# Optimization experiments

Measured on AMD Instinct MI355X. Metric: run time of the kernel, lower is better.

## Reference

```python
import jax, jax.numpy as jnp
import numpy as np

B, N, F_IN, H, L = 4, 2048, 3, 32, 3
H2 = H // 2


def setup_inputs() -> dict:
    key = jax.random.key(0)
    ks = jax.random.split(key, 16)
    feats = jax.random.normal(ks[0], (B, N, F_IN), dtype=jnp.float32)
    coors = jax.random.normal(ks[1], (B, N, 3), dtype=jnp.float32) * 3.0
    adj = jax.random.randint(ks[2], (B, N, N), 0, 2).astype(bool)
    adj = adj | jnp.eye(N, dtype=bool)[None]  # self-loops so every row has a neighbor
    s = 0.1
    return {
        "feats": feats,
        "coors": coors,
        "adj_mat": adj,
        "W_in": jax.random.normal(ks[3], (F_IN, H), dtype=jnp.float32) * s,
        "Wq": jax.random.normal(ks[4], (L, H, H), dtype=jnp.float32) * s,
        "Wk": jax.random.normal(ks[5], (L, H, H), dtype=jnp.float32) * s,
        "Wv": jax.random.normal(ks[6], (L, H, H), dtype=jnp.float32) * s,
        "Wo": jax.random.normal(ks[7], (L, H, H), dtype=jnp.float32) * s,
        "W1": jax.random.normal(ks[8], (L, H, 2 * H), dtype=jnp.float32) * s,
        "W2": jax.random.normal(ks[9], (L, 2 * H, H), dtype=jnp.float32) * s,
        "coor_scale": jnp.full((L,), 0.1, dtype=jnp.float32),
        "Wf1": jax.random.normal(ks[10], (H, H2), dtype=jnp.float32) * s,
        "bf1": jnp.zeros((H2,), dtype=jnp.float32),
        "Wf2": jax.random.normal(ks[11], (H2, 3), dtype=jnp.float32) * s,
        "bf2": jnp.zeros((3,), dtype=jnp.float32),
    }


def _se3_forward(feats, coors, adj_mat, W_in, Wq, Wk, Wv, Wo, W1, W2, coor_scale):
    h = feats @ W_in                      # [B,N,H]
    x = coors
    neg = jnp.finfo(h.dtype).min
    inv_sqrt_d = 1.0 / jnp.sqrt(jnp.asarray(H, h.dtype))
    for l in range(L):                    # small static layer loop
        rel = x[:, :, None, :] - x[:, None, :, :]          # [B,N,N,3]
        dist2 = jnp.sum(rel * rel, axis=-1)                 # [B,N,N]
        q = h @ Wq[l]
        k = h @ Wk[l]
        v = h @ Wv[l]
        logits = jnp.einsum('bie,bje->bij', q, k) * inv_sqrt_d - dist2
        logits = jnp.where(adj_mat, logits, neg)
        attn = jax.nn.softmax(logits, axis=-1)              # [B,N,N]
        h = h + jnp.einsum('bij,bjd->bid', attn, v) @ Wo[l]
        # equivariant coordinate update (attention-weighted relative vectors)
        x = x + coor_scale[l] * jnp.einsum('bij,bijc->bic', attn, rel)
        h = h + jax.nn.relu(h @ W1[l]) @ W2[l]
    return h


def reference(feats, coors, adj_mat, W_in, Wq, Wk, Wv, Wo, W1, W2,
              coor_scale, Wf1, bf1, Wf2, bf2):
    h = _se3_forward(feats, coors, adj_mat, W_in, Wq, Wk, Wv, Wo, W1, W2, coor_scale)
    pooled = h.mean(axis=1)                                 # [B,H]
    out = jax.nn.relu(pooled @ Wf1 + bf1) @ Wf2 + bf2       # [B,3]
    return out
```

## Files before the change

kernel.cpp:

```cpp
#include <hip/hip_runtime.h>
#include <cstddef>
#include <cstdint>

#define N_     2048
#define H_     32
#define NEGF   (-1.0e30f)
#define LOG2E  1.4426950408889634f
#define C1F    (0.17677669529663687f * 1.4426950408889634f)
#define DEFER  16.0f
#define NCHUNK 32
#define CLEN   64
#define NRTOT  8192
#define PREC   20

#define AS1 __attribute__((address_space(1)))
#define AS3 __attribute__((address_space(3)))

typedef unsigned short ushortT;
typedef short v8s __attribute__((ext_vector_type(8)));
typedef float v4f __attribute__((ext_vector_type(4)));

__device__ __forceinline__ float exp2_fast(float x) {
    float r;
    asm("v_exp_f32 %0, %1" : "=v"(r) : "v"(x));
    return r;
}

__device__ __forceinline__ unsigned f2bf(float x) {
    unsigned u = __builtin_bit_cast(unsigned, x);
    return (u + 0x7FFFu + ((u >> 16) & 1u)) >> 16;
}

__global__ __launch_bounds__(256) void k_adjmask(const int* __restrict__ adj,
                                                 unsigned long long* __restrict__ mask) {
    size_t idx = (size_t)blockIdx.x * 256 + threadIdx.x;
    unsigned long long m = __ballot(adj[idx] != 0);
    if ((threadIdx.x & 63) == 0) mask[idx >> 6] = m;
}

__global__ __launch_bounds__(256) void k_init_qkv(const float* __restrict__ feats,
                                                  const float* __restrict__ W_in,
                                                  const float* __restrict__ Wq,
                                                  const float* __restrict__ Wk,
                                                  const float* __restrict__ Wv,
                                                  float* __restrict__ h,
                                                  ushortT* __restrict__ qb,
                                                  ushortT* __restrict__ kb,
                                                  ushortT* __restrict__ vb) {
    __shared__ float hs[8][33];
    int t = threadIdx.x;
    int rl = t >> 5, c = t & 31;
    int row = blockIdx.x * 8 + rl;
    float f0 = feats[row * 3 + 0], f1 = feats[row * 3 + 1], f2 = feats[row * 3 + 2];
    float hv = f0 * W_in[c] + f1 * W_in[32 + c] + f2 * W_in[64 + c];
    hs[rl][c] = hv;
    h[(row << 5) + c] = hv;
    __syncthreads();
    float aq = 0.f, ak = 0.f, av = 0.f;
#pragma unroll
    for (int d = 0; d < 32; ++d) {
        float hd = hs[rl][d];
        aq += hd * Wq[(d << 5) + c];
        ak += hd * Wk[(d << 5) + c];
        av += hd * Wv[(d << 5) + c];
    }
    qb[(row << 5) + c] = (ushortT)f2bf(aq * C1F);
    kb[(row << 5) + c] = (ushortT)f2bf(ak);
    vb[(row << 5) + c] = (ushortT)f2bf(av);
}

__global__ __launch_bounds__(256) void k_attn(const ushortT* __restrict__ qb,
                                              const ushortT* __restrict__ kb,
                                              const ushortT* __restrict__ vb,
                                              const float* __restrict__ xin,
                                              const unsigned long long* __restrict__ maskg,
                                              float* __restrict__ pm,
                                              float* __restrict__ ps,
                                              unsigned* __restrict__ pacc) {
    __shared__ __attribute__((aligned(16))) ushortT k_lds[64 * 32];
    __shared__ __attribute__((aligned(16))) ushortT vt_lds[32 * 72];
    __shared__ __attribute__((aligned(16))) float4  x_lds[64];
    __shared__ __attribute__((aligned(16))) ushortT p_lds[4][16 * 40];

    const int t = threadIdx.x;
    const int w = t >> 6, l = t & 63;
    const int g = l >> 4, q = l & 15;
    const int rowblk = blockIdx.x >> 5;
    const int cid    = blockIdx.x & 31;
    const int bN = (rowblk >> 5) << 11;
    const int j0 = cid << 6;
    const int rq = rowblk * 64 + w * 16 + q;

    __builtin_amdgcn_global_load_lds(
        (const AS1 void*)((const char*)(kb + (((size_t)(bN + j0)) << 5)) + t * 16),
        (AS3 void*)((char*)k_lds + t * 16), 16, 0, 0);
    {
        const int j = t & 63, grp = t >> 6;
        const uint4 vv = *(const uint4*)(vb + (((size_t)(bN + j0 + j)) << 5) + grp * 8);
        unsigned arr[4] = {vv.x, vv.y, vv.z, vv.w};
#pragma unroll
        for (int ii = 0; ii < 4; ++ii) {
            vt_lds[(grp * 8 + 2 * ii) * 72 + j]     = (ushortT)(arr[ii] & 0xffffu);
            vt_lds[(grp * 8 + 2 * ii + 1) * 72 + j] = (ushortT)(arr[ii] >> 16);
        }
    }
    if (t < 64) {
        const float* xp = xin + ((size_t)(bN + j0 + t)) * 3;
        float4 xv; xv.x = xp[0]; xv.y = xp[1]; xv.z = xp[2]; xv.w = 0.f;
        x_lds[t] = xv;
    }

    const v8s qf = *(const v8s*)(qb + (((size_t)rq) << 5) + g * 8);
    const float xi0 = xin[rq * 3 + 0], xi1 = xin[rq * 3 + 1], xi2 = xin[rq * 3 + 2];
    const unsigned long long mw = maskg[(((size_t)rq) << 5) + cid];

    v4f oA = {0.f, 0.f, 0.f, 0.f}, oB = {0.f, 0.f, 0.f, 0.f};
    float m = NEGF, sum = 0.f;
    float xa0 = 0.f, xa1 = 0.f, xa2 = 0.f;

    __syncthreads();

    ushortT* pw = &p_lds[w][0];

#pragma unroll
    for (int half = 0; half < 2; ++half) {
        const int jt = half * 32;
        v8s kA = *(const v8s*)(k_lds + (jt + q) * 32 + g * 8);
        v8s kB = *(const v8s*)(k_lds + (jt + 16 + q) * 32 + g * 8);
        v4f zero = {0.f, 0.f, 0.f, 0.f};
        v4f sA = __builtin_amdgcn_mfma_f32_16x16x32_bf16(kA, qf, zero, 0, 0, 0);
        v4f sB = __builtin_amdgcn_mfma_f32_16x16x32_bf16(kB, qf, zero, 0, 0, 0);

        float se[8];
        float4 xjA[4], xjB[4];
        float pot = NEGF;
#pragma unroll
        for (int reg = 0; reg < 4; ++reg) {
            const int jA = jt + 4 * g + reg, jB = jA + 16;
            xjA[reg] = x_lds[jA];
            xjB[reg] = x_lds[jB];
            float dA0 = xi0 - xjA[reg].x, dA1 = xi1 - xjA[reg].y, dA2 = xi2 - xjA[reg].z;
            float dB0 = xi0 - xjB[reg].x, dB1 = xi1 - xjB[reg].y, dB2 = xi2 - xjB[reg].z;
            float distA = fmaf(dA2, dA2, fmaf(dA1, dA1, dA0 * dA0));
            float distB = fmaf(dB2, dB2, fmaf(dB1, dB1, dB0 * dB0));
            const int bA = (int)((mw >> jA) & 1ULL);
            const int bB = (int)((mw >> jB) & 1ULL);
            se[reg]     = bA ? fmaf(distA, -LOG2E, sA[reg]) : NEGF;
            se[4 + reg] = bB ? fmaf(distB, -LOG2E, sB[reg]) : NEGF;
            pot = fmaxf(pot, fmaxf(se[reg], se[4 + reg]));
        }
        pot = fmaxf(pot, __shfl_xor(pot, 16));
        pot = fmaxf(pot, __shfl_xor(pot, 32));
        if (__any(pot - m > DEFER)) {
            float n2 = fmaxf(m, pot);
            float al = exp2_fast(m - n2);
            m = n2; sum *= al;
            v4f alv = {al, al, al, al};
            oA *= alv; oB *= alv;
            xa0 *= al; xa1 *= al; xa2 *= al;
        }
        float p[8];
#pragma unroll
        for (int i = 0; i < 8; ++i) { p[i] = exp2_fast(se[i] - m); sum += p[i]; }
#pragma unroll
        for (int reg = 0; reg < 4; ++reg) {
            xa0 = fmaf(p[reg], xjA[reg].x, fmaf(p[4 + reg], xjB[reg].x, xa0));
            xa1 = fmaf(p[reg], xjA[reg].y, fmaf(p[4 + reg], xjB[reg].y, xa1));
            xa2 = fmaf(p[reg], xjA[reg].z, fmaf(p[4 + reg], xjB[reg].z, xa2));
        }
        uint2 wA, wB;
        wA.x = f2bf(p[0]) | (f2bf(p[1]) << 16);
        wA.y = f2bf(p[2]) | (f2bf(p[3]) << 16);
        wB.x = f2bf(p[4]) | (f2bf(p[5]) << 16);
        wB.y = f2bf(p[6]) | (f2bf(p[7]) << 16);
        *(uint2*)(pw + q * 40 + 4 * g)      = wA;
        *(uint2*)(pw + q * 40 + 16 + 4 * g) = wB;
        v8s pf = *(const v8s*)(pw + q * 40 + 8 * g);
        v8s vA = *(const v8s*)(vt_lds + q * 72 + jt + 8 * g);
        v8s vB = *(const v8s*)(vt_lds + (16 + q) * 72 + jt + 8 * g);
        oA = __builtin_amdgcn_mfma_f32_16x16x32_bf16(vA, pf, oA, 0, 0, 0);
        oB = __builtin_amdgcn_mfma_f32_16x16x32_bf16(vB, pf, oB, 0, 0, 0);
    }

    sum += __shfl_xor(sum, 16); sum += __shfl_xor(sum, 32);
    xa0 += __shfl_xor(xa0, 16); xa0 += __shfl_xor(xa0, 32);
    xa1 += __shfl_xor(xa1, 16); xa1 += __shfl_xor(xa1, 32);
    xa2 += __shfl_xor(xa2, 16); xa2 += __shfl_xor(xa2, 32);

    unsigned* pb = pacc + ((size_t)cid * NRTOT + rq) * PREC;
    uint2 rA, rB;
    rA.x = f2bf(oA[0]) | (f2bf(oA[1]) << 16);
    rA.y = f2bf(oA[2]) | (f2bf(oA[3]) << 16);
    rB.x = f2bf(oB[0]) | (f2bf(oB[1]) << 16);
    rB.y = f2bf(oB[2]) | (f2bf(oB[3]) << 16);
    *(uint2*)(pb + 2 * g)     = rA;
    *(uint2*)(pb + 8 + 2 * g) = rB;
    if (g == 0) {
        float4 tl; tl.x = xa0; tl.y = xa1; tl.z = xa2; tl.w = 0.f;
        *(float4*)(pb + 16) = tl;
        pm[(((size_t)rq) << 5) + cid] = m;
        ps[(((size_t)rq) << 5) + cid] = sum;
    }
}

__global__ __launch_bounds__(256) void k_mergefin(const float* __restrict__ pm,
                                                  const float* __restrict__ ps,
                                                  const unsigned* __restrict__ pacc,
                                                  float* __restrict__ hg,
                                                  const float* __restrict__ xin,
                                                  float* __restrict__ xout,
                                                  const float* __restrict__ Wo,
                                                  const float* __restrict__ W1,
                                                  const float* __restrict__ W2,
                                                  const float* __restrict__ csp,
                                                  const float* __restrict__ Wqn,
                                                  const float* __restrict__ Wkn,
                                                  const float* __restrict__ Wvn,
                                                  ushortT* __restrict__ qout,
                                                  ushortT* __restrict__ kout,
                                                  ushortT* __restrict__ vout) {
    __shared__ float wo_s[1024];
    __shared__ float w1_s[2048];
    __shared__ float w2_s[2048];
    __shared__ float wq_s[1024];
    __shared__ float wk_s[1024];
    __shared__ float wv_s[1024];
    __shared__ float ad_s[4][40];
    __shared__ float h1_s[4][36];
    __shared__ float h2_s[4][36];
    __shared__ float f_s[4][64];

    const int t = threadIdx.x, w = t >> 6, lane = t & 63;
    for (int i = t; i < 1024; i += 256) wo_s[i] = Wo[i];
    for (int i = t; i < 2048; i += 256) { w1_s[i] = W1[i]; w2_s[i] = W2[i]; }
    if (Wqn) {
        for (int i = t; i < 1024; i += 256) {
            wq_s[i] = Wqn[i]; wk_s[i] = Wkn[i]; wv_s[i] = Wvn[i];
        }
    }
    __syncthreads();

    const int r = (blockIdx.x << 2) + w;

    float pmv = NEGF, psv = 0.f;
    if (lane < NCHUNK) { pmv = pm[((size_t)r << 5) + lane]; psv = ps[((size_t)r << 5) + lane]; }
    float m_g = pmv;
#pragma unroll
    for (int off = 1; off < 64; off <<= 1) m_g = fmaxf(m_g, __shfl_xor(m_g, off));
    float scv = (lane < NCHUNK) ? exp2_fast(pmv - m_g) : 0.f;
    float sg = scv * psv;
#pragma unroll
    for (int off = 1; off < 64; off <<= 1) sg += __shfl_xor(sg, off);
    const float rinv = 1.0f / sg;

    const int off32 = (lane < 32) ? (lane >> 1) : (16 + ((lane - 32) & 3));
    const bool isTail = lane >= 32;
    const bool hiHalf = lane & 1;
    float ad = 0.f;
#pragma unroll
    for (int c = 0; c < NCHUNK; ++c) {
        float scc = __shfl(scv, c);
        unsigned u = pacc[((size_t)c * NRTOT + r) * PREC + off32];
        float f = isTail ? __builtin_bit_cast(float, u)
                         : __builtin_bit_cast(float, hiHalf ? (u & 0xffff0000u) : (u << 16));
        ad = fmaf(scc, f, ad);
    }
    if (lane < 35) ad_s[w][lane] = ad;

    const int col = lane & 31;
    float hv = 0.f;
#pragma unroll
    for (int d = 0; d < 32; ++d) hv = fmaf(ad_s[w][d], wo_s[(d << 5) + col], hv);
    float h1 = 0.f;
    if (lane < 32) { h1 = hg[(((size_t)r) << 5) + lane] + hv * rinv; h1_s[w][lane] = h1; }

    float f = 0.f;
#pragma unroll
    for (int d = 0; d < 32; ++d) f = fmaf(h1_s[w][d], w1_s[(d << 6) + lane], f);
    f = fmaxf(f, 0.f);
    f_s[w][lane] = f;

    if (lane < 32) {
        float v2a = 0.f;
#pragma unroll
        for (int u = 0; u < 64; ++u) v2a = fmaf(f_s[w][u], w2_s[(u << 5) + lane], v2a);
        float hnew = h1 + v2a;
        hg[(((size_t)r) << 5) + lane] = hnew;
        h2_s[w][lane] = hnew;
    }

    if (lane < 3) {
        float o  = ad_s[w][32 + lane] * rinv;
        float xi = xin[r * 3 + lane];
        xout[r * 3 + lane] = xi + csp[0] * (xi - o);
    }

    if (Wqn && lane < 32) {
        float aq = 0.f, ak = 0.f, av = 0.f;
#pragma unroll
        for (int d = 0; d < 32; ++d) {
            float hd = h2_s[w][d];
            aq = fmaf(hd, wq_s[(d << 5) + lane], aq);
            ak = fmaf(hd, wk_s[(d << 5) + lane], ak);
            av = fmaf(hd, wv_s[(d << 5) + lane], av);
        }
        qout[(((size_t)r) << 5) + lane] = (ushortT)f2bf(aq * C1F);
        kout[(((size_t)r) << 5) + lane] = (ushortT)f2bf(ak);
        vout[(((size_t)r) << 5) + lane] = (ushortT)f2bf(av);
    }
}

__global__ __launch_bounds__(256) void k_pool(const float* __restrict__ h,
                                              float* __restrict__ pool_ws) {
    const int b = blockIdx.x >> 5, sub = blockIdx.x & 31;
    const int t = threadIdx.x, c = t & 31, g = t >> 5;
    float s = 0.f;
#pragma unroll
    for (int i = 0; i < 8; ++i) {
        int row = (sub << 6) + (g << 3) + i;
        s += h[(((size_t)((b << 11) + row)) << 5) + c];
    }
    __shared__ float pool[8][32];
    pool[g][c] = s;
    __syncthreads();
    if (t < 32) {
        float ss = 0.f;
#pragma unroll
        for (int gg = 0; gg < 8; ++gg) ss += pool[gg][t];
        pool_ws[((b << 5) + sub) * 32 + t] = ss;
    }
}

__global__ __launch_bounds__(256) void k_head(const float* __restrict__ pool_ws,
                                              const float* __restrict__ Wf1,
                                              const float* __restrict__ bf1,
                                              const float* __restrict__ Wf2,
                                              const float* __restrict__ bf2,
                                              float* __restrict__ out) {
    __shared__ float pooled[4][32];
    __shared__ float a1[4][16];
    const int t = threadIdx.x;
    if (t < 128) {
        int b = t >> 5, c = t & 31;
        float ss = 0.f;
#pragma unroll
        for (int sub = 0; sub < 32; ++sub) ss += pool_ws[((b << 5) + sub) * 32 + c];
        pooled[b][c] = ss * (1.0f / N_);
    }
    __syncthreads();
    if (t < 64) {
        int b = t >> 4, u = t & 15;
        float a = bf1[u];
#pragma unroll
        for (int d = 0; d < 32; ++d) a += pooled[b][d] * Wf1[(d << 4) + u];
        a1[b][u] = fmaxf(a, 0.f);
    }
    __syncthreads();
    if (t < 12) {
        int b = t / 3, o = t - b * 3;
        float v = bf2[o];
#pragma unroll
        for (int e = 0; e < 16; ++e) v += a1[b][e] * Wf2[e * 3 + o];
        out[b * 3 + o] = v;
    }
}

extern "C" void kernel_launch(void* const* d_in, const int* in_sizes, int n_in,
                              void* d_out, int out_size, void* d_ws, size_t ws_size,
                              hipStream_t stream) {
    const float* feats = (const float*)d_in[0];
    const float* coors = (const float*)d_in[1];
    const int*   adj   = (const int*)d_in[2];
    const float* W_in  = (const float*)d_in[3];
    const float* Wq    = (const float*)d_in[4];
    const float* Wk    = (const float*)d_in[5];
    const float* Wv    = (const float*)d_in[6];
    const float* Wo    = (const float*)d_in[7];
    const float* W1    = (const float*)d_in[8];
    const float* W2    = (const float*)d_in[9];
    const float* csc   = (const float*)d_in[10];
    const float* Wf1   = (const float*)d_in[11];
    const float* bf1   = (const float*)d_in[12];
    const float* Wf2   = (const float*)d_in[13];
    const float* bf2   = (const float*)d_in[14];

    const size_t BNH = (size_t)4 * N_ * H_;
    float* ws = (float*)d_ws;
    float* h  = ws;
    ushortT* qb = (ushortT*)(ws + BNH);
    ushortT* kb = qb + BNH;
    ushortT* vb = kb + BNH;
    float* x0 = (float*)(vb + BNH);
    float* x1 = x0 + (size_t)4 * N_ * 3;
    unsigned long long* mask = (unsigned long long*)(x1 + (size_t)4 * N_ * 3);
    float* pm   = (float*)(mask + 262144);
    float* ps   = pm + (size_t)NCHUNK * NRTOT;
    unsigned* pacc = (unsigned*)(ps + (size_t)NCHUNK * NRTOT);
    float* pool_ws = (float*)(pacc + (size_t)NCHUNK * NRTOT * PREC);

    k_adjmask<<<65536, 256, 0, stream>>>(adj, mask);
    k_init_qkv<<<1024, 256, 0, stream>>>(feats, W_in, Wq, Wk, Wv, h, qb, kb, vb);

    const float* xin[3]  = {coors, x0, x1};
    float*       xout[3] = {x0, x1, x0};
    for (int l = 0; l < 3; ++l) {
        k_attn<<<4096, 256, 0, stream>>>(qb, kb, vb, xin[l], mask, pm, ps, pacc);
        const bool last = (l == 2);
        k_mergefin<<<2048, 256, 0, stream>>>(pm, ps, pacc, h, xin[l], xout[l],
                                             Wo + l * 1024, W1 + l * 2048, W2 + l * 2048,
                                             csc + l,
                                             last ? nullptr : Wq + (l + 1) * 1024,
                                             last ? nullptr : Wk + (l + 1) * 1024,
                                             last ? nullptr : Wv + (l + 1) * 1024,
                                             qb, kb, vb);
    }
    k_pool<<<128, 256, 0, stream>>>(h, pool_ws);
    k_head<<<1, 256, 0, stream>>>(pool_ws, Wf1, bf1, Wf2, bf2, (float*)d_out);
}
```

Baseline: 154.8 us.

## Widen attention key chunks to 256 with double-buffered LDS staging

Each attention block now handles 256 keys as four 64-key tiles instead of one 64-key chunk. The K, V and x tiles are double-buffered in LDS so the next tile is loaded while the current one is computed. Split-softmax partials drop from 32 to 8 per row, which shrinks the partial-buffer traffic and the merge work in k_mergefin. The cost is a quarter as many blocks (1024), so there is less parallelism, plus a barrier after every tile.

```diff
diff --git a/kernel.cpp b/kernel.cpp
--- a/kernel.cpp
+++ b/kernel.cpp
@@ -8,8 +8,8 @@
 #define LOG2E  1.4426950408889634f
 #define C1F    (0.17677669529663687f * 1.4426950408889634f)
 #define DEFER  16.0f
-#define NCHUNK 32
-#define CLEN   64
+#define NCHUNK 8
+#define CLEN   256
 #define NRTOT  8192
 #define PREC   20
 
@@ -77,110 +77,122 @@
                                               float* __restrict__ pm,
                                               float* __restrict__ ps,
                                               unsigned* __restrict__ pacc) {
-    __shared__ __attribute__((aligned(16))) ushortT k_lds[64 * 32];
-    __shared__ __attribute__((aligned(16))) ushortT vt_lds[32 * 72];
-    __shared__ __attribute__((aligned(16))) float4  x_lds[64];
+    __shared__ __attribute__((aligned(16))) ushortT k_lds[2][64 * 32];
+    __shared__ __attribute__((aligned(16))) ushortT vt_lds[2][32 * 72];
+    __shared__ __attribute__((aligned(16))) float4  x_lds[2][64];
     __shared__ __attribute__((aligned(16))) ushortT p_lds[4][16 * 40];
 
     const int t = threadIdx.x;
     const int w = t >> 6, l = t & 63;
     const int g = l >> 4, q = l & 15;
-    const int rowblk = blockIdx.x >> 5;
-    const int cid    = blockIdx.x & 31;
+    const int rowblk = blockIdx.x >> 3;
+    const int cid    = blockIdx.x & 7;
     const int bN = (rowblk >> 5) << 11;
-    const int j0 = cid << 6;
+    const int j0 = cid << 8;
     const int rq = rowblk * 64 + w * 16 + q;
 
-    __builtin_amdgcn_global_load_lds(
-        (const AS1 void*)((const char*)(kb + (((size_t)(bN + j0)) << 5)) + t * 16),
-        (AS3 void*)((char*)k_lds + t * 16), 16, 0, 0);
-    {
-        const int j = t & 63, grp = t >> 6;
-        const uint4 vv = *(const uint4*)(vb + (((size_t)(bN + j0 + j)) << 5) + grp * 8);
-        unsigned arr[4] = {vv.x, vv.y, vv.z, vv.w};
-#pragma unroll
-        for (int ii = 0; ii < 4; ++ii) {
-            vt_lds[(grp * 8 + 2 * ii) * 72 + j]     = (ushortT)(arr[ii] & 0xffffu);
-            vt_lds[(grp * 8 + 2 * ii + 1) * 72 + j] = (ushortT)(arr[ii] >> 16);
-        }
-    }
-    if (t < 64) {
-        const float* xp = xin + ((size_t)(bN + j0 + t)) * 3;
-        float4 xv; xv.x = xp[0]; xv.y = xp[1]; xv.z = xp[2]; xv.w = 0.f;
-        x_lds[t] = xv;
-    }
+#define STAGE_TILE(BUF, TILE)                                                                  \
+    do {                                                                                       \
+        const int jj0 = (TILE) << 6;                                                           \
+        __builtin_amdgcn_global_load_lds(                                                      \
+            (const AS1 void*)((const char*)(kb + (((size_t)(bN + j0 + jj0)) << 5)) + t * 16),  \
+            (AS3 void*)((char*)&k_lds[BUF][0] + t * 16), 16, 0, 0);                            \
+        const int j_ = t & 63, grp_ = t >> 6;                                                  \
+        const uint4 vv = *(const uint4*)(vb + (((size_t)(bN + j0 + jj0 + j_)) << 5) + grp_ * 8);\
+        unsigned arr[4] = {vv.x, vv.y, vv.z, vv.w};                                            \
+        _Pragma("unroll")                                                                      \
+        for (int ii = 0; ii < 4; ++ii) {                                                       \
+            vt_lds[BUF][(grp_ * 8 + 2 * ii) * 72 + j_]     = (ushortT)(arr[ii] & 0xffffu);     \
+            vt_lds[BUF][(grp_ * 8 + 2 * ii + 1) * 72 + j_] = (ushortT)(arr[ii] >> 16);         \
+        }                                                                                      \
+        if (t < 64) {                                                                          \
+            const float* xp_ = xin + ((size_t)(bN + j0 + jj0 + t)) * 3;                        \
+            float4 xv_; xv_.x = xp_[0]; xv_.y = xp_[1]; xv_.z = xp_[2]; xv_.w = 0.f;           \
+            x_lds[BUF][t] = xv_;                                                               \
+        }                                                                                      \
+    } while (0)
 
     const v8s qf = *(const v8s*)(qb + (((size_t)rq) << 5) + g * 8);
     const float xi0 = xin[rq * 3 + 0], xi1 = xin[rq * 3 + 1], xi2 = xin[rq * 3 + 2];
-    const unsigned long long mw = maskg[(((size_t)rq) << 5) + cid];
 
     v4f oA = {0.f, 0.f, 0.f, 0.f}, oB = {0.f, 0.f, 0.f, 0.f};
     float m = NEGF, sum = 0.f;
     float xa0 = 0.f, xa1 = 0.f, xa2 = 0.f;
 
-    __syncthreads();
-
     ushortT* pw = &p_lds[w][0];
 
-#pragma unroll
-    for (int half = 0; half < 2; ++half) {
-        const int jt = half * 32;
-        v8s kA = *(const v8s*)(k_lds + (jt + q) * 32 + g * 8);
-        v8s kB = *(const v8s*)(k_lds + (jt + 16 + q) * 32 + g * 8);
-        v4f zero = {0.f, 0.f, 0.f, 0.f};
-        v4f sA = __builtin_amdgcn_mfma_f32_16x16x32_bf16(kA, qf, zero, 0, 0, 0);
-        v4f sB = __builtin_amdgcn_mfma_f32_16x16x32_bf16(kB, qf, zero, 0, 0, 0);
-
-        float se[8];
-        float4 xjA[4], xjB[4];
-        float pot = NEGF;
-#pragma unroll
-        for (int reg = 0; reg < 4; ++reg) {
-            const int jA = jt + 4 * g + reg, jB = jA + 16;
-            xjA[reg] = x_lds[jA];
-            xjB[reg] = x_lds[jB];
-            float dA0 = xi0 - xjA[reg].x, dA1 = xi1 - xjA[reg].y, dA2 = xi2 - xjA[reg].z;
-            float dB0 = xi0 - xjB[reg].x, dB1 = xi1 - xjB[reg].y, dB2 = xi2 - xjB[reg].z;
-            float distA = fmaf(dA2, dA2, fmaf(dA1, dA1, dA0 * dA0));
-            float distB = fmaf(dB2, dB2, fmaf(dB1, dB1, dB0 * dB0));
-            const int bA = (int)((mw >> jA) & 1ULL);
-            const int bB = (int)((mw >> jB) & 1ULL);
-            se[reg]     = bA ? fmaf(distA, -LOG2E, sA[reg]) : NEGF;
-            se[4 + reg] = bB ? fmaf(distB, -LOG2E, sB[reg]) : NEGF;
-            pot = fmaxf(pot, fmaxf(se[reg], se[4 + reg]));
+    STAGE_TILE(0, 0);
+    __syncthreads();
+
+    int cur = 0;
+#pragma unroll
+    for (int tile = 0; tile < 4; ++tile) {
+        if (tile < 3) STAGE_TILE(cur ^ 1, tile + 1);
+        const unsigned long long mw = maskg[(((size_t)rq) << 5) + (cid << 2) + tile];
+
+#pragma unroll
+        for (int half = 0; half < 2; ++half) {
+            const int jt = half * 32;
+            v8s kA = *(const v8s*)(&k_lds[cur][0] + (jt + q) * 32 + g * 8);
+            v8s kB = *(const v8s*)(&k_lds[cur][0] + (jt + 16 + q) * 32 + g * 8);
+            v4f zero = {0.f, 0.f, 0.f, 0.f};
+            v4f sA = __builtin_amdgcn_mfma_f32_16x16x32_bf16(kA, qf, zero, 0, 0, 0);
+            v4f sB = __builtin_amdgcn_mfma_f32_16x16x32_bf16(kB, qf, zero, 0, 0, 0);
+
+            float se[8];
+            float4 xjA[4], xjB[4];
+            float pot = NEGF;
+#pragma unroll
+            for (int reg = 0; reg < 4; ++reg) {
+                const int jA = jt + 4 * g + reg, jB = jA + 16;
+                xjA[reg] = x_lds[cur][jA];
+                xjB[reg] = x_lds[cur][jB];
+                float dA0 = xi0 - xjA[reg].x, dA1 = xi1 - xjA[reg].y, dA2 = xi2 - xjA[reg].z;
+                float dB0 = xi0 - xjB[reg].x, dB1 = xi1 - xjB[reg].y, dB2 = xi2 - xjB[reg].z;
+                float distA = fmaf(dA2, dA2, fmaf(dA1, dA1, dA0 * dA0));
+                float distB = fmaf(dB2, dB2, fmaf(dB1, dB1, dB0 * dB0));
+                const int bA = (int)((mw >> jA) & 1ULL);
+                const int bB = (int)((mw >> jB) & 1ULL);
+                se[reg]     = bA ? fmaf(distA, -LOG2E, sA[reg]) : NEGF;
+                se[4 + reg] = bB ? fmaf(distB, -LOG2E, sB[reg]) : NEGF;
+                pot = fmaxf(pot, fmaxf(se[reg], se[4 + reg]));
+            }
+            pot = fmaxf(pot, __shfl_xor(pot, 16));
+            pot = fmaxf(pot, __shfl_xor(pot, 32));
+            if (__any(pot - m > DEFER)) {
+                float n2 = fmaxf(m, pot);
+                float al = exp2_fast(m - n2);
+                m = n2; sum *= al;
+                v4f alv = {al, al, al, al};
+                oA *= alv; oB *= alv;
+                xa0 *= al; xa1 *= al; xa2 *= al;
+            }
+            float p[8];
+#pragma unroll
+            for (int i = 0; i < 8; ++i) { p[i] = exp2_fast(se[i] - m); sum += p[i]; }
+#pragma unroll
+            for (int reg = 0; reg < 4; ++reg) {
+                xa0 = fmaf(p[reg], xjA[reg].x, fmaf(p[4 + reg], xjB[reg].x, xa0));
+                xa1 = fmaf(p[reg], xjA[reg].y, fmaf(p[4 + reg], xjB[reg].y, xa1));
+                xa2 = fmaf(p[reg], xjA[reg].z, fmaf(p[4 + reg], xjB[reg].z, xa2));
+            }
+            uint2 wA, wB;
+            wA.x = f2bf(p[0]) | (f2bf(p[1]) << 16);
+            wA.y = f2bf(p[2]) | (f2bf(p[3]) << 16);
+            wB.x = f2bf(p[4]) | (f2bf(p[5]) << 16);
+            wB.y = f2bf(p[6]) | (f2bf(p[7]) << 16);
+            *(uint2*)(pw + q * 40 + 4 * g)      = wA;
+            *(uint2*)(pw + q * 40 + 16 + 4 * g) = wB;
+            v8s pf = *(const v8s*)(pw + q * 40 + 8 * g);
+            v8s vA = *(const v8s*)(&vt_lds[cur][0] + q * 72 + jt + 8 * g);
+            v8s vB = *(const v8s*)(&vt_lds[cur][0] + (16 + q) * 72 + jt + 8 * g);
+            oA = __builtin_amdgcn_mfma_f32_16x16x32_bf16(vA, pf, oA, 0, 0, 0);
+            oB = __builtin_amdgcn_mfma_f32_16x16x32_bf16(vB, pf, oB, 0, 0, 0);
         }
-        pot = fmaxf(pot, __shfl_xor(pot, 16));
-        pot = fmaxf(pot, __shfl_xor(pot, 32));
-        if (__any(pot - m > DEFER)) {
-            float n2 = fmaxf(m, pot);
-            float al = exp2_fast(m - n2);
-            m = n2; sum *= al;
-            v4f alv = {al, al, al, al};
-            oA *= alv; oB *= alv;
-            xa0 *= al; xa1 *= al; xa2 *= al;
-        }
-        float p[8];
-#pragma unroll
-        for (int i = 0; i < 8; ++i) { p[i] = exp2_fast(se[i] - m); sum += p[i]; }
-#pragma unroll
-        for (int reg = 0; reg < 4; ++reg) {
-            xa0 = fmaf(p[reg], xjA[reg].x, fmaf(p[4 + reg], xjB[reg].x, xa0));
-            xa1 = fmaf(p[reg], xjA[reg].y, fmaf(p[4 + reg], xjB[reg].y, xa1));
-            xa2 = fmaf(p[reg], xjA[reg].z, fmaf(p[4 + reg], xjB[reg].z, xa2));
-        }
-        uint2 wA, wB;
-        wA.x = f2bf(p[0]) | (f2bf(p[1]) << 16);
-        wA.y = f2bf(p[2]) | (f2bf(p[3]) << 16);
-        wB.x = f2bf(p[4]) | (f2bf(p[5]) << 16);
-        wB.y = f2bf(p[6]) | (f2bf(p[7]) << 16);
-        *(uint2*)(pw + q * 40 + 4 * g)      = wA;
-        *(uint2*)(pw + q * 40 + 16 + 4 * g) = wB;
-        v8s pf = *(const v8s*)(pw + q * 40 + 8 * g);
-        v8s vA = *(const v8s*)(vt_lds + q * 72 + jt + 8 * g);
-        v8s vB = *(const v8s*)(vt_lds + (16 + q) * 72 + jt + 8 * g);
-        oA = __builtin_amdgcn_mfma_f32_16x16x32_bf16(vA, pf, oA, 0, 0, 0);
-        oB = __builtin_amdgcn_mfma_f32_16x16x32_bf16(vB, pf, oB, 0, 0, 0);
-    }
+        __syncthreads();
+        cur ^= 1;
+    }
+#undef STAGE_TILE
 
     sum += __shfl_xor(sum, 16); sum += __shfl_xor(sum, 32);
     xa0 += __shfl_xor(xa0, 16); xa0 += __shfl_xor(xa0, 32);
@@ -198,8 +210,8 @@
     if (g == 0) {
         float4 tl; tl.x = xa0; tl.y = xa1; tl.z = xa2; tl.w = 0.f;
         *(float4*)(pb + 16) = tl;
-        pm[(((size_t)rq) << 5) + cid] = m;
-        ps[(((size_t)rq) << 5) + cid] = sum;
+        pm[(((size_t)rq) << 3) + cid] = m;
+        ps[(((size_t)rq) << 3) + cid] = sum;
     }
 }
 
@@ -243,7 +255,7 @@
     const int r = (blockIdx.x << 2) + w;
 
     float pmv = NEGF, psv = 0.f;
-    if (lane < NCHUNK) { pmv = pm[((size_t)r << 5) + lane]; psv = ps[((size_t)r << 5) + lane]; }
+    if (lane < NCHUNK) { pmv = pm[((size_t)r << 3) + lane]; psv = ps[((size_t)r << 3) + lane]; }
     float m_g = pmv;
 #pragma unroll
     for (int off = 1; off < 64; off <<= 1) m_g = fmaxf(m_g, __shfl_xor(m_g, off));
@@ -404,7 +416,7 @@
     const float* xin[3]  = {coors, x0, x1};
     float*       xout[3] = {x0, x1, x0};
     for (int l = 0; l < 3; ++l) {
-        k_attn<<<4096, 256, 0, stream>>>(qb, kb, vb, xin[l], mask, pm, ps, pacc);
+        k_attn<<<1024, 256, 0, stream>>>(qb, kb, vb, xin[l], mask, pm, ps, pacc);
         const bool last = (l == 2);
         k_mergefin<<<2048, 256, 0, stream>>>(pm, ps, pacc, h, xin[l], xout[l],
                                              Wo + l * 1024, W1 + l * 2048, W2 + l * 2048,
```

Result: faster. 148.8 us (-3.9%).
